# Optimization experiments

Measured on AMD Instinct MI355X. Metric: run time of the kernel, lower is better.

Reference implementation:

```python
import jax, jax.numpy as jnp
import numpy as np

D_MODEL = 1024
NUM_HEADS = 16
D_K = D_MODEL // NUM_HEADS
SCALE = float(np.sqrt(D_K))


def setup_inputs() -> dict:
    key = jax.random.key(0)
    ks = jax.random.split(key, 11)
    B, S = 2, 2048
    s = 0.02
    return {
        "query": jax.random.normal(ks[0], (B, S, D_MODEL), dtype=jnp.float32),
        "key_in": jax.random.normal(ks[1], (B, S, D_MODEL), dtype=jnp.float32),
        "value": jax.random.normal(ks[2], (B, S, D_MODEL), dtype=jnp.float32),
        "w_q": jax.random.normal(ks[3], (D_MODEL, D_MODEL), dtype=jnp.float32) * s,
        "b_q": jnp.zeros((D_MODEL,), dtype=jnp.float32),
        "w_k": jax.random.normal(ks[4], (D_MODEL, D_MODEL), dtype=jnp.float32) * s,
        "b_k": jnp.zeros((D_MODEL,), dtype=jnp.float32),
        "w_v": jax.random.normal(ks[5], (D_MODEL, D_MODEL), dtype=jnp.float32) * s,
        "b_v": jnp.zeros((D_MODEL,), dtype=jnp.float32),
        "w_o": jax.random.normal(ks[6], (D_MODEL, D_MODEL), dtype=jnp.float32) * s,
        "b_o": jnp.zeros((D_MODEL,), dtype=jnp.float32),
    }


def _mha(query, key_in, value, w_q, b_q, w_k, b_k, w_v, b_v, w_o, b_o):
    B, S, _ = query.shape
    # linear projections (x @ W + b), split into heads: [B, H, S, Dk]
    def proj(x, w, b):
        y = x @ w + b
        return y.reshape(B, -1, NUM_HEADS, D_K).transpose(0, 2, 1, 3)

    Q = proj(query, w_q, b_q)
    K = proj(key_in, w_k, b_k)
    V = proj(value, w_v, b_v)

    # scores: [B, H, Sq, Sk]
    scores = jnp.einsum("bhqd,bhkd->bhqk", Q, K) / SCALE
    attn = jax.nn.softmax(scores, axis=-1)  # dropout is identity in eval mode
    out = jnp.einsum("bhqk,bhkd->bhqd", attn, V)
    out = out.transpose(0, 2, 1, 3).reshape(B, S, D_MODEL)
    return out @ w_o + b_o


def reference(query, key_in, value, w_q, b_q, w_k, b_k, w_v, b_v, w_o, b_o):
    return _mha(query, key_in, value, w_q, b_q, w_k, b_k, w_v, b_v, w_o, b_o)
```

## Files before the change

### kernel.cpp

```cpp
#include <hip/hip_runtime.h>
#include <cstdint>

#define S_LEN 2048
#define DMODEL 1024
#define NHEADS 16
#define DK 64
#define BATCH 2
#define M_TOT 4096

typedef __attribute__((ext_vector_type(8)))  short  short8;
typedef __attribute__((ext_vector_type(4)))  float  f32x4;
typedef __attribute__((ext_vector_type(16))) float  f32x16;

__device__ __forceinline__ ushort f2bf(float f) {
    union { float f; uint32_t u; } v; v.f = f;
    uint32_t r = (v.u + 0x7fffu + ((v.u >> 16) & 1u)) >> 16;
    return (ushort)r;
}
__device__ __forceinline__ float bf2f(ushort u) {
    union { uint32_t u; float f; } v; v.u = ((uint32_t)u) << 16;
    return v.f;
}
__device__ __forceinline__ float max3f(float a, float b, float c) {
    float d;
    asm("v_max3_f32 %0, %1, %2, %3" : "=v"(d) : "v"(a), "v"(b), "v"(c));
    return d;
}

__device__ __forceinline__ void gl_lds16(const void* g, void* l) {
    __builtin_amdgcn_global_load_lds(
        (const __attribute__((address_space(1))) void*)(g),
        (__attribute__((address_space(3))) void*)(l), 16, 0, 0);
}

__global__ __launch_bounds__(256)
void conv3_kernel(const float* __restrict__ a0, const float* __restrict__ a1,
                  const float* __restrict__ a2, ushort* __restrict__ o0,
                  ushort* __restrict__ o1, ushort* __restrict__ o2, int n8)
{
    const float*  in  = blockIdx.z == 0 ? a0 : (blockIdx.z == 1 ? a1 : a2);
    ushort*       out = blockIdx.z == 0 ? o0 : (blockIdx.z == 1 ? o1 : o2);
    int i = blockIdx.x * 256 + threadIdx.x;
    const int stride = gridDim.x * 256;
    for (; i < n8; i += stride) {
        const float4* p = (const float4*)(in + (size_t)i * 8);
        float4 a = p[0], b = p[1];
        ushort r[8];
        r[0]=f2bf(a.x); r[1]=f2bf(a.y); r[2]=f2bf(a.z); r[3]=f2bf(a.w);
        r[4]=f2bf(b.x); r[5]=f2bf(b.y); r[6]=f2bf(b.z); r[7]=f2bf(b.w);
        *(ushort4*)(out + (size_t)i * 8)     = *(ushort4*)&r[0];
        *(ushort4*)(out + (size_t)i * 8 + 4) = *(ushort4*)&r[4];
    }
}

__global__ __launch_bounds__(256)
void wtrans4_kernel(const float* __restrict__ wq, const float* __restrict__ wk,
                    const float* __restrict__ wv, const float* __restrict__ wo,
                    ushort* __restrict__ oq, ushort* __restrict__ ok,
                    ushort* __restrict__ ov, ushort* __restrict__ oo_hi,
                    ushort* __restrict__ oo_lo)
{
    const int z = blockIdx.z;
    const float* w  = z == 0 ? wq : (z == 1 ? wk : (z == 2 ? wv : wo));
    ushort*      hi = z == 0 ? oq : (z == 1 ? ok : (z == 2 ? ov : oo_hi));
    const bool   LO = (z == 3);

    __shared__ float t[64][65];
    const int n0 = blockIdx.x * 64, k0 = blockIdx.y * 64;
    const int r  = threadIdx.x >> 2;
    const int cb = (threadIdx.x & 3) * 16;

    #pragma unroll
    for (int j = 0; j < 4; ++j) {
        float4 v = *(const float4*)(w + (size_t)(k0 + r) * DMODEL + n0 + cb + j * 4);
        t[r][cb + j*4 + 0] = v.x;
        t[r][cb + j*4 + 1] = v.y;
        t[r][cb + j*4 + 2] = v.z;
        t[r][cb + j*4 + 3] = v.w;
    }
    __syncthreads();

    ushort h8[16], l8[16];
    #pragma unroll
    for (int j = 0; j < 16; ++j) {
        float x = t[cb + j][r];
        ushort h = f2bf(x);
        h8[j] = h;
        l8[j] = f2bf(x - bf2f(h));
    }
    ushort* dsth = hi + (size_t)(n0 + r) * DMODEL + k0 + cb;
    #pragma unroll
    for (int j = 0; j < 4; ++j)
        *(ushort4*)(dsth + j*4) = *(ushort4*)&h8[j*4];
    if (LO) {
        ushort* dstl = oo_lo + (size_t)(n0 + r) * DMODEL + k0 + cb;
        #pragma unroll
        for (int j = 0; j < 4; ++j)
            *(ushort4*)(dstl + j*4) = *(ushort4*)&l8[j*4];
    }
}

__global__ __launch_bounds__(256)
void gemm_qkv_kernel(const ushort* __restrict__ Aq, const ushort* __restrict__ Ak,
                     const ushort* __restrict__ Av, const ushort* __restrict__ Wq,
                     const ushort* __restrict__ Wk, const ushort* __restrict__ Wv,
                     const float* __restrict__ bq, const float* __restrict__ bk,
                     const float* __restrict__ bv, ushort* __restrict__ Qh,
                     ushort* __restrict__ Kh, ushort* __restrict__ Vt, float qscale)
{
    const int z = blockIdx.z;
    const ushort* A    = z == 0 ? Aq : (z == 1 ? Ak : Av);
    const ushort* Bt   = z == 0 ? Wq : (z == 1 ? Wk : Wv);
    const float*  bias = z == 0 ? bq : (z == 1 ? bk : bv);
    ushort*       out  = z == 0 ? Qh : (z == 1 ? Kh : Vt);
    const float oscale = z == 0 ? qscale : 1.0f;
    const int   mode   = z == 2 ? 2 : 1;

    __shared__ __align__(16) ushort lds[2][12288];

    const int t = threadIdx.x, wv = t >> 6, lane = t & 63;
    const int c = lane & 15, g = lane >> 4;
    const int m0 = blockIdx.y * 128, n0 = blockIdx.x * 64;
    const int wr = wv >> 1, wc = wv & 1;
    const int lrow = lane >> 3, lcol = lane & 7;

    f32x4 acc[4][2];
    #pragma unroll
    for (int i = 0; i < 4; ++i)
        #pragma unroll
        for (int j = 0; j < 2; ++j)
            acc[i][j] = (f32x4){0.f, 0.f, 0.f, 0.f};

    auto stage = [&](int buf, int kt) {
        #pragma unroll
        for (int j = 0; j < 6; ++j) {
            const int ci = wv * 6 + j;
            ushort* dst = &lds[buf][ci * 512];
            const ushort* src;
            if (ci < 16) {
                const int row  = ci * 8 + lrow;
                const int colb = (lcol * 16) ^ ((row & 7) << 4);
                src = A + (size_t)(m0 + row) * 1024 + kt * 64 + (colb >> 1);
            } else {
                const int row  = (ci - 16) * 8 + lrow;
                const int colb = (lcol * 16) ^ ((row & 7) << 4);
                src = Bt + (size_t)(n0 + row) * 1024 + kt * 64 + (colb >> 1);
            }
            gl_lds16(src, dst);
        }
    };

    stage(0, 0);
    __syncthreads();

    for (int kt = 0; kt < 16; ++kt) {
        const int cur = kt & 1;
        if (kt < 15) stage(cur ^ 1, kt + 1);

        const char* la = (const char*)&lds[cur][0];
        const char* lb = (const char*)&lds[cur][8192];
        #pragma unroll
        for (int kk = 0; kk < 2; ++kk) {
            short8 af[4], bf[2];
            #pragma unroll
            for (int mf = 0; mf < 4; ++mf) {
                const int row = wr * 64 + mf * 16 + c;
                af[mf] = *(const short8*)(la + row * 128 +
                          ((kk * 64 + g * 16) ^ ((c & 7) << 4)));
            }
            #pragma unroll
            for (int nf = 0; nf < 2; ++nf) {
                const int row = wc * 32 + nf * 16 + c;
                bf[nf] = *(const short8*)(lb + row * 128 +
                          ((kk * 64 + g * 16) ^ ((c & 7) << 4)));
            }
            #pragma unroll
            for (int mf = 0; mf < 4; ++mf)
                #pragma unroll
                for (int nf = 0; nf < 2; ++nf)
                    acc[mf][nf] = __builtin_amdgcn_mfma_f32_16x16x32_bf16(
                        af[mf], bf[nf], acc[mf][nf], 0, 0, 0);
        }
        __syncthreads();
    }

    const int b      = m0 >> 11;
    const int s_base = m0 & 2047;
    #pragma unroll
    for (int nf = 0; nf < 2; ++nf) {
        const int ncol = n0 + wc * 32 + nf * 16 + c;
        const float bv = bias[ncol];
        const int h = ncol >> 6, dk = ncol & 63;
        #pragma unroll
        for (int mf = 0; mf < 4; ++mf) {
            if (mode == 1) {
                #pragma unroll
                for (int j = 0; j < 4; ++j) {
                    const int s = s_base + wr * 64 + mf * 16 + g * 4 + j;
                    out[(((size_t)(b * NHEADS + h) * S_LEN + s) * DK) + dk] =
                        f2bf((acc[mf][nf][j] + bv) * oscale);
                }
            } else {
                ushort4 v4;
                v4.x = f2bf(acc[mf][nf][0] + bv);
                v4.y = f2bf(acc[mf][nf][1] + bv);
                v4.z = f2bf(acc[mf][nf][2] + bv);
                v4.w = f2bf(acc[mf][nf][3] + bv);
                const int s = s_base + wr * 64 + mf * 16 + g * 4;
                *(ushort4*)&out[((size_t)(b * NHEADS + h) * DK + dk) * S_LEN + s] = v4;
            }
        }
    }
}

__global__ __launch_bounds__(256)
void gemm_o2_kernel(const ushort* __restrict__ A, const ushort* __restrict__ Bhi,
                    const ushort* __restrict__ Blo, const float* __restrict__ bias,
                    float* __restrict__ out)
{
    __shared__ __align__(16) ushort lds[2][16384];

    const int t = threadIdx.x, wv = t >> 6, lane = t & 63;
    const int c = lane & 15, g = lane >> 4;
    const int m0 = blockIdx.y * 128, n0 = blockIdx.x * 64;
    const int wr = wv >> 1, wc = wv & 1;
    const int lrow = lane >> 3, lcol = lane & 7;

    f32x4 acc[4][2];
    #pragma unroll
    for (int i = 0; i < 4; ++i)
        #pragma unroll
        for (int j = 0; j < 2; ++j)
            acc[i][j] = (f32x4){0.f, 0.f, 0.f, 0.f};

    auto stage = [&](int buf, int kt) {
        #pragma unroll
        for (int j = 0; j < 8; ++j) {
            const int ci = wv * 8 + j;
            ushort* dst = &lds[buf][ci * 512];
            const ushort* src;
            if (ci < 16) {
                const int row  = ci * 8 + lrow;
                const int colb = (lcol * 16) ^ ((row & 7) << 4);
                src = A + (size_t)(m0 + row) * 1024 + kt * 64 + (colb >> 1);
            } else if (ci < 24) {
                const int row  = (ci - 16) * 8 + lrow;
                const int colb = (lcol * 16) ^ ((row & 7) << 4);
                src = Bhi + (size_t)(n0 + row) * 1024 + kt * 64 + (colb >> 1);
            } else {
                const int row  = (ci - 24) * 8 + lrow;
                const int colb = (lcol * 16) ^ ((row & 7) << 4);
                src = Blo + (size_t)(n0 + row) * 1024 + kt * 64 + (colb >> 1);
            }
            gl_lds16(src, dst);
        }
    };

    stage(0, 0);
    __syncthreads();

    for (int kt = 0; kt < 16; ++kt) {
        const int cur = kt & 1;
        if (kt < 15) stage(cur ^ 1, kt + 1);

        const char* la = (const char*)&lds[cur][0];
        const char* lh = (const char*)&lds[cur][8192];
        const char* ll = (const char*)&lds[cur][12288];
        #pragma unroll
        for (int kk = 0; kk < 2; ++kk) {
            short8 af[4], bh[2], bl[2];
            #pragma unroll
            for (int mf = 0; mf < 4; ++mf) {
                const int row = wr * 64 + mf * 16 + c;
                af[mf] = *(const short8*)(la + row * 128 +
                          ((kk * 64 + g * 16) ^ ((c & 7) << 4)));
            }
            #pragma unroll
            for (int nf = 0; nf < 2; ++nf) {
                const int row = wc * 32 + nf * 16 + c;
                const int off = row * 128 + ((kk * 64 + g * 16) ^ ((c & 7) << 4));
                bh[nf] = *(const short8*)(lh + off);
                bl[nf] = *(const short8*)(ll + off);
            }
            #pragma unroll
            for (int mf = 0; mf < 4; ++mf)
                #pragma unroll
                for (int nf = 0; nf < 2; ++nf) {
                    acc[mf][nf] = __builtin_amdgcn_mfma_f32_16x16x32_bf16(af[mf], bh[nf], acc[mf][nf], 0,0,0);
                    acc[mf][nf] = __builtin_amdgcn_mfma_f32_16x16x32_bf16(af[mf], bl[nf], acc[mf][nf], 0,0,0);
                }
        }
        __syncthreads();
    }

    #pragma unroll
    for (int nf = 0; nf < 2; ++nf) {
        const int ncol = n0 + wc * 32 + nf * 16 + c;
        const float bv = bias[ncol];
        #pragma unroll
        for (int mf = 0; mf < 4; ++mf)
            #pragma unroll
            for (int j = 0; j < 4; ++j) {
                const int m = m0 + wr * 64 + mf * 16 + g * 4 + j;
                out[(size_t)m * 1024 + ncol] = acc[mf][nf][j] + bv;
            }
    }
}

__global__ __launch_bounds__(256, 2)
void attn_kernel5(const ushort* __restrict__ Qh, const ushort* __restrict__ Kh,
                  const ushort* __restrict__ Vt, ushort* __restrict__ ctx)
{
    __shared__ __align__(16) ushort KV[2][8192];

    const int t  = threadIdx.x, wv = t >> 6, lane = t & 63;
    const int q  = lane & 31;
    const int hi = lane >> 5;
    const int bh = blockIdx.y;
    const int q0 = blockIdx.x * 128 + wv * 32;

    const ushort* Kb = Kh + (size_t)bh * S_LEN * DK;
    const ushort* Vb = Vt + (size_t)bh * DK * S_LEN;
    const ushort* Qb = Qh + ((size_t)bh * S_LEN + q0 + q) * DK;

    short8 qf[4];
    #pragma unroll
    for (int s = 0; s < 4; ++s)
        qf[s] = *(const short8*)(Qb + s * 16 + hi * 8);

    const ushort* sbase[4];
    int sstr[4];
    char* dbase[4];
    #pragma unroll
    for (int j = 0; j < 4; ++j) {
        const int D = (j * 256 + t) * 16;
        dbase[j] = (char*)&KV[0][0] + D;
        if (D < 8192) {
            const int row = D >> 7;
            const int X   = D & 127;
            const int Xs  = X ^ ((((row & 7) ^ ((row >> 3) & 3))) << 4);
            sbase[j] = Kb + row * DK + (Xs >> 1);
            sstr[j]  = DK;
        } else {
            const int Y   = D - 8192;
            const int kk  = Y >> 12;
            const int Z   = Y & 4095;
            const int r   = Z >> 7;
            const int gsl = ((Z & 127) >> 4) ^ ((r & 7) ^ ((r >> 3) & 3));
            const int d   = r + ((gsl >> 2) << 5);
            sbase[j] = Vb + (size_t)d * S_LEN + kk * 32 + (gsl & 3) * 8;
            sstr[j]  = 1;
        }
    }
    auto stage = [&](int buf, int k0) {
        #pragma unroll
        for (int j = 0; j < 4; ++j)
            gl_lds16(sbase[j] + (size_t)k0 * sstr[j], dbase[j] + buf * 16384);
    };

    float m = -3.0e38f, l = 0.f;
    f32x16 accO[2];
    #pragma unroll
    for (int i = 0; i < 16; ++i) { accO[0][i] = 0.f; accO[1][i] = 0.f; }

    const int swz = ((q & 7) ^ ((q >> 3) & 3)) << 4;

    stage(0, 0);
    __syncthreads();

    for (int kt = 0; kt < 32; ++kt) {
        const int cur = kt & 1;
        if (kt < 31) stage(cur ^ 1, (kt + 1) * 64);

        const char* Kl = (const char*)&KV[cur][0];
        const char* Vl = Kl + 8192;

        #pragma unroll
        for (int kk = 0; kk < 2; ++kk) {
            f32x16 sa;
            #pragma unroll
            for (int i = 0; i < 16; ++i) sa[i] = 0.f;
            #pragma unroll
            for (int s = 0; s < 4; ++s) {
                short8 kf = *(const short8*)(Kl + (kk * 32 + q) * 128 +
                                             ((s * 32 + hi * 16) ^ swz));
                sa = __builtin_amdgcn_mfma_f32_32x32x16_bf16(kf, qf[s], sa, 0, 0, 0);
            }

            float m0_ = max3f(sa[0],  sa[1],  sa[2]);
            float m1_ = max3f(sa[3],  sa[4],  sa[5]);
            float m2_ = max3f(sa[6],  sa[7],  sa[8]);
            float m3_ = max3f(sa[9],  sa[10], sa[11]);
            float m4_ = max3f(sa[12], sa[13], sa[14]);
            float mt  = fmaxf(max3f(m0_, m1_, m2_), max3f(m3_, m4_, sa[15]));
            mt = fmaxf(mt, __shfl_xor(mt, 32));

            if (__any(mt > m + 8.f)) {
                const float mnew = fmaxf(m, mt);
                const float corr = __builtin_amdgcn_exp2f(m - mnew);
                #pragma unroll
                for (int r = 0; r < 16; ++r) { accO[0][r] *= corr; accO[1][r] *= corr; }
                l *= corr;
                m = mnew;
            }

            float p[16], ps = 0.f;
            #pragma unroll
            for (int r = 0; r < 16; ++r) {
                p[r] = __builtin_amdgcn_exp2f(sa[r] - m);
                ps += p[r];
            }
            ps += __shfl_xor(ps, 32);
            l += ps;

            uint32_t u[8];
            #pragma unroll
            for (int jj = 0; jj < 8; ++jj)
                asm("v_cvt_pk_bf16_f32 %0, %1, %2"
                    : "=v"(u[jj]) : "v"(p[2*jj]), "v"(p[2*jj+1]));
            asm("v_permlane32_swap_b32 %0, %1" : "+v"(u[0]), "+v"(u[2]));
            asm("v_permlane32_swap_b32 %0, %1" : "+v"(u[1]), "+v"(u[3]));
            asm("v_permlane32_swap_b32 %0, %1" : "+v"(u[4]), "+v"(u[6]));
            asm("v_permlane32_swap_b32 %0, %1" : "+v"(u[5]), "+v"(u[7]));
            union { uint32_t w[4]; short8 s8; } pb0, pb1;
            pb0.w[0]=u[0]; pb0.w[1]=u[1]; pb0.w[2]=u[2]; pb0.w[3]=u[3];
            pb1.w[0]=u[4]; pb1.w[1]=u[5]; pb1.w[2]=u[6]; pb1.w[3]=u[7];

            const char* Vg = Vl + kk * 4096;
            #pragma unroll
            for (int db = 0; db < 2; ++db) {
                short8 vf0 = *(const short8*)(Vg + q * 128 + ((db*64 +      hi*16) ^ swz));
                short8 vf1 = *(const short8*)(Vg + q * 128 + ((db*64 + 32 + hi*16) ^ swz));
                accO[db] = __builtin_amdgcn_mfma_f32_32x32x16_bf16(vf0, pb0.s8, accO[db], 0, 0, 0);
                accO[db] = __builtin_amdgcn_mfma_f32_32x32x16_bf16(vf1, pb1.s8, accO[db], 0, 0, 0);
            }
        }
        __syncthreads();
    }

    const float inv = 1.f / l;
    const int b = bh >> 4, h = bh & 15;
    ushort* base = ctx + ((size_t)b * S_LEN + q0 + q) * DMODEL + h * DK;
    #pragma unroll
    for (int db = 0; db < 2; ++db)
        #pragma unroll
        for (int r = 0; r < 16; ++r) {
            const int d = db * 32 + (r & 3) + 8 * (r >> 2) + 4 * hi;
            base[d] = f2bf(accO[db][r] * inv);
        }
}

extern "C" void kernel_launch(void* const* d_in, const int* in_sizes, int n_in,
                              void* d_out, int out_size, void* d_ws, size_t ws_size,
                              hipStream_t stream)
{
    const float* query  = (const float*)d_in[0];
    const float* key_in = (const float*)d_in[1];
    const float* value  = (const float*)d_in[2];
    const float* w_q = (const float*)d_in[3];
    const float* b_q = (const float*)d_in[4];
    const float* w_k = (const float*)d_in[5];
    const float* b_k = (const float*)d_in[6];
    const float* w_v = (const float*)d_in[7];
    const float* b_v = (const float*)d_in[8];
    const float* w_o = (const float*)d_in[9];
    const float* b_o = (const float*)d_in[10];
    float* out = (float*)d_out;

    const size_t E4M = (size_t)M_TOT * DMODEL;
    const size_t E1M = (size_t)DMODEL * DMODEL;

    ushort* ws = (ushort*)d_ws;
    ushort* Aq    = ws;
    ushort* Ak    = Aq + E4M;
    ushort* Av    = Ak + E4M;
    ushort* Qh    = Av + E4M;
    ushort* Kh    = Qh + E4M;
    ushort* Vt    = Kh + E4M;
    ushort* Wq    = Vt + E4M;
    ushort* Wk    = Wq + E1M;
    ushort* Wv    = Wk + E1M;
    ushort* Wo_hi = Wv + E1M;
    ushort* Wo_lo = Wo_hi + E1M;
    ushort* ctx   = Aq;

    const float qscale = 0.125f * 1.44269504088896340736f;

    dim3 blk(256);
    hipLaunchKernelGGL(conv3_kernel, dim3(512, 1, 3), blk, 0, stream,
                       query, key_in, value, Aq, Ak, Av, (int)(E4M / 8));
    hipLaunchKernelGGL(wtrans4_kernel, dim3(16, 16, 4), blk, 0, stream,
                       w_q, w_k, w_v, w_o, Wq, Wk, Wv, Wo_hi, Wo_lo);

    dim3 ggrd(DMODEL / 64, M_TOT / 128, 3);
    hipLaunchKernelGGL(gemm_qkv_kernel, ggrd, blk, 0, stream,
                       Aq, Ak, Av, Wq, Wk, Wv, b_q, b_k, b_v, Qh, Kh, Vt, qscale);

    dim3 agrd(S_LEN / 128, BATCH * NHEADS);
    hipLaunchKernelGGL(attn_kernel5, agrd, blk, 0, stream, Qh, Kh, Vt, ctx);

    dim3 ogrd(DMODEL / 64, M_TOT / 128);
    hipLaunchKernelGGL(gemm_o2_kernel, ogrd, blk, 0, stream,
                       ctx, Wo_hi, Wo_lo, b_o, out);
}
```

Baseline: 130.3 us.

## Split attention over key range with separate softmax-merge combine kernel

Splits each attention block's key sequence into two halves processed by separate blocks, saving partial normalized outputs plus per-row max and sum. A new combine kernel rescales and merges the two partials into the context buffer. The intent is more parallelism and better CU utilization for attention, at the cost of an extra kernel launch, extra global traffic for partial outputs, and an added bf16 rounding of partial results.

```diff
diff --git a/kernel.cpp b/kernel.cpp
--- a/kernel.cpp
+++ b/kernel.cpp
@@ -7,6 +7,8 @@
 #define DK 64
 #define BATCH 2
 #define M_TOT 4096
+#define NSPLIT 2
+#define BHS (BATCH * NHEADS * S_LEN)
 
 typedef __attribute__((ext_vector_type(8)))  short  short8;
 typedef __attribute__((ext_vector_type(4)))  float  f32x4;
@@ -308,8 +310,9 @@
 }
 
 __global__ __launch_bounds__(256, 2)
-void attn_kernel5(const ushort* __restrict__ Qh, const ushort* __restrict__ Kh,
-                  const ushort* __restrict__ Vt, ushort* __restrict__ ctx)
+void attn_split_kernel(const ushort* __restrict__ Qh, const ushort* __restrict__ Kh,
+                       const ushort* __restrict__ Vt, ushort* __restrict__ Op,
+                       float* __restrict__ msave, float* __restrict__ lsave)
 {
     __shared__ __align__(16) ushort KV[2][8192];
 
@@ -318,6 +321,8 @@
     const int hi = lane >> 5;
     const int bh = blockIdx.y;
     const int q0 = blockIdx.x * 128 + wv * 32;
+    const int split = blockIdx.z;
+    const int kbase = split * (S_LEN / NSPLIT);
 
     const ushort* Kb = Kh + (size_t)bh * S_LEN * DK;
     const ushort* Vb = Vt + (size_t)bh * DK * S_LEN;
@@ -365,12 +370,13 @@
 
     const int swz = ((q & 7) ^ ((q >> 3) & 3)) << 4;
 
-    stage(0, 0);
+    stage(0, kbase);
     __syncthreads();
 
-    for (int kt = 0; kt < 32; ++kt) {
+    const int NT = S_LEN / NSPLIT / 64;
+    for (int kt = 0; kt < NT; ++kt) {
         const int cur = kt & 1;
-        if (kt < 31) stage(cur ^ 1, (kt + 1) * 64);
+        if (kt < NT - 1) stage(cur ^ 1, kbase + (kt + 1) * 64);
 
         const char* Kl = (const char*)&KV[cur][0];
         const char* Vl = Kl + 8192;
@@ -439,8 +445,8 @@
     }
 
     const float inv = 1.f / l;
-    const int b = bh >> 4, h = bh & 15;
-    ushort* base = ctx + ((size_t)b * S_LEN + q0 + q) * DMODEL + h * DK;
+    const size_t sIdx = ((size_t)split * BATCH * NHEADS + bh) * S_LEN + q0 + q;
+    ushort* base = Op + sIdx * DK;
     #pragma unroll
     for (int db = 0; db < 2; ++db)
         #pragma unroll
@@ -448,6 +454,51 @@
             const int d = db * 32 + (r & 3) + 8 * (r >> 2) + 4 * hi;
             base[d] = f2bf(accO[db][r] * inv);
         }
+    if (hi == 0) {
+        msave[sIdx] = m;
+        lsave[sIdx] = l;
+    }
+}
+
+__global__ __launch_bounds__(256)
+void combine_kernel(const ushort* __restrict__ Op, const float* __restrict__ msave,
+                    const float* __restrict__ lsave, ushort* __restrict__ ctx)
+{
+    const int idx = blockIdx.x * 256 + threadIdx.x;
+    const int bh = idx >> 11;
+    const int s  = idx & 2047;
+
+    const float m1 = msave[idx],        l1 = lsave[idx];
+    const float m2 = msave[BHS + idx],  l2 = lsave[BHS + idx];
+    const float mmax = fmaxf(m1, m2);
+    const float w1 = l1 * __builtin_amdgcn_exp2f(m1 - mmax);
+    const float w2 = l2 * __builtin_amdgcn_exp2f(m2 - mmax);
+    const float inv = 1.f / (w1 + w2);
+    const float r1 = w1 * inv, r2 = w2 * inv;
+
+    const ushort* o1 = Op + (size_t)idx * DK;
+    const ushort* o2 = Op + ((size_t)BHS + idx) * DK;
+    const int b = bh >> 4, h = bh & 15;
+    ushort* dst = ctx + ((size_t)b * S_LEN + s) * DMODEL + h * DK;
+
+    #pragma unroll
+    for (int j = 0; j < 8; ++j) {
+        ushort4 a = *(const ushort4*)(o1 + j * 8);
+        ushort4 bq = *(const ushort4*)(o1 + j * 8 + 4);
+        ushort4 c = *(const ushort4*)(o2 + j * 8);
+        ushort4 dq = *(const ushort4*)(o2 + j * 8 + 4);
+        ushort r[8];
+        r[0] = f2bf(r1 * bf2f(a.x) + r2 * bf2f(c.x));
+        r[1] = f2bf(r1 * bf2f(a.y) + r2 * bf2f(c.y));
+        r[2] = f2bf(r1 * bf2f(a.z) + r2 * bf2f(c.z));
+        r[3] = f2bf(r1 * bf2f(a.w) + r2 * bf2f(c.w));
+        r[4] = f2bf(r1 * bf2f(bq.x) + r2 * bf2f(dq.x));
+        r[5] = f2bf(r1 * bf2f(bq.y) + r2 * bf2f(dq.y));
+        r[6] = f2bf(r1 * bf2f(bq.z) + r2 * bf2f(dq.z));
+        r[7] = f2bf(r1 * bf2f(bq.w) + r2 * bf2f(dq.w));
+        *(ushort4*)(dst + j * 8)     = *(ushort4*)&r[0];
+        *(ushort4*)(dst + j * 8 + 4) = *(ushort4*)&r[4];
+    }
 }
 
 extern "C" void kernel_launch(void* const* d_in, const int* in_sizes, int n_in,
@@ -482,7 +533,10 @@
     ushort* Wv    = Wk + E1M;
     ushort* Wo_hi = Wv + E1M;
     ushort* Wo_lo = Wo_hi + E1M;
+    float*  msave = (float*)(Wo_lo + E1M);
+    float*  lsave = msave + (size_t)NSPLIT * BHS;
     ushort* ctx   = Aq;
+    ushort* Op    = Ak;
 
     const float qscale = 0.125f * 1.44269504088896340736f;
 
@@ -496,8 +550,12 @@
     hipLaunchKernelGGL(gemm_qkv_kernel, ggrd, blk, 0, stream,
                        Aq, Ak, Av, Wq, Wk, Wv, b_q, b_k, b_v, Qh, Kh, Vt, qscale);
 
-    dim3 agrd(S_LEN / 128, BATCH * NHEADS);
-    hipLaunchKernelGGL(attn_kernel5, agrd, blk, 0, stream, Qh, Kh, Vt, ctx);
+    dim3 agrd(S_LEN / 128, BATCH * NHEADS, NSPLIT);
+    hipLaunchKernelGGL(attn_split_kernel, agrd, blk, 0, stream,
+                       Qh, Kh, Vt, Op, msave, lsave);
+
+    hipLaunchKernelGGL(combine_kernel, dim3(BHS / 256), blk, 0, stream,
+                       Op, msave, lsave, ctx);
 
     dim3 ogrd(DMODEL / 64, M_TOT / 128);
     hipLaunchKernelGGL(gemm_o2_kernel, ogrd, blk, 0, stream,
```

Measured after the change: 138.2 us. 1.06x slower.
